# Kernel optimization log

Measured on AMD Instinct MI355X. Metric: run time of the kernel, lower is better.

Reference implementation:

```python
import jax, jax.numpy as jnp
import numpy as np

DIST_THRESHOLD = 900.0  # distance_threshold from __init__
NO_CODE_ID = -1         # no_code_id from __init__


def setup_inputs() -> dict:
    key = jax.random.key(0)
    k1, k2 = jax.random.split(key)
    x = jax.random.normal(k1, (4, 2048, 512), dtype=jnp.float32)      # [b, n, d] tokens
    codes = jax.random.normal(k2, (16384, 512), dtype=jnp.float32)    # [c, d] full codebook
    return {"x": x, "codes": codes}


def reference(x, codes):
    x2 = jnp.sum(x * x, axis=-1, keepdims=True)            # [b, n, 1]
    c2 = jnp.sum(codes * codes, axis=-1)                   # [c]
    xc = jnp.einsum('bnd,cd->bnc', x, codes)               # [b, n, c] (the compute-heavy GEMM)
    dist_sq = jnp.maximum(x2 + c2 - 2.0 * xc, 0.0)         # clamp tiny negatives, like cdist

    within = jnp.any(dist_sq <= DIST_THRESHOLD, axis=-1)   # [b, n]
    nn_ids = jnp.argmin(dist_sq, axis=-1)                  # [b, n]
    ids = jnp.where(within, nn_ids, NO_CODE_ID)            # tokens outside threshold -> no_code_id
    return ids
```

## Files before the change

### kernel.cpp

```cpp
#include <hip/hip_runtime.h>


#define NTOK   8192
#define NCODES 16384
#define DDIM   512
#define NCHUNK 8
#define CHUNK  2048
#define DIST_THR 900.0f

typedef unsigned short u16;
typedef _Float16 half8 __attribute__((ext_vector_type(8)));
typedef float    f32x4 __attribute__((ext_vector_type(4)));

__device__ __forceinline__ void conv_body(const float* __restrict__ src,
                                          u16* __restrict__ dh,
                                          u16* __restrict__ dl, int c) {
    int r = c & 15, q = (c >> 4) & 3, g = (c >> 6) & 7, kit = (c >> 9) & 15;
    int tile = c >> 13;
    int row = tile * 128 + g * 16 + r;
    int k = kit * 32 + q * 8;
    const float* p = src + (size_t)row * DDIM + k;
    float4 v0 = *(const float4*)p;
    float4 v1 = *(const float4*)(p + 4);
    float vv[8] = {v0.x, v0.y, v0.z, v0.w, v1.x, v1.y, v1.z, v1.w};
    u16 hs[8], ls[8];
    #pragma unroll
    for (int j = 0; j < 8; ++j) {
        float sv = vv[j] * 16.0f;
        _Float16 h = (_Float16)sv;
        float hf = (float)h;
        _Float16 l = (_Float16)(sv - hf);
        union { _Float16 f; u16 u; } uh, ul;
        uh.f = h; ul.f = l;
        hs[j] = uh.u; ls[j] = ul.u;
    }
    uint4 H, L;
    H.x = hs[0] | ((unsigned)hs[1] << 16); H.y = hs[2] | ((unsigned)hs[3] << 16);
    H.z = hs[4] | ((unsigned)hs[5] << 16); H.w = hs[6] | ((unsigned)hs[7] << 16);
    L.x = ls[0] | ((unsigned)ls[1] << 16); L.y = ls[2] | ((unsigned)ls[3] << 16);
    L.z = ls[4] | ((unsigned)ls[5] << 16); L.w = ls[6] | ((unsigned)ls[7] << 16);
    *(uint4*)(dh + (size_t)c * 8) = H;
    *(uint4*)(dl + (size_t)c * 8) = L;
}

__global__ __launch_bounds__(256) void nn_prep(const float* __restrict__ x,
                                               const float* __restrict__ codes,
                                               u16* __restrict__ xh, u16* __restrict__ xl,
                                               u16* __restrict__ ch, u16* __restrict__ cl,
                                               float* __restrict__ c2) {
    int b = blockIdx.x;
    if (b < 2048) {
        conv_body(x, xh, xl, b * 256 + threadIdx.x);
    } else if (b < 6144) {
        conv_body(codes, ch, cl, (b - 2048) * 256 + threadIdx.x);
    } else {
        int w = threadIdx.x >> 6;
        int lane = threadIdx.x & 63;
        int c = (b - 6144) * 4 + w;
        const float* p = codes + (size_t)c * DDIM + lane * 8;
        float4 v0 = *(const float4*)p;
        float4 v1 = *(const float4*)(p + 4);
        float s = v0.x*v0.x + v0.y*v0.y + v0.z*v0.z + v0.w*v0.w
                + v1.x*v1.x + v1.y*v1.y + v1.z*v1.z + v1.w*v1.w;
        #pragma unroll
        for (int off = 32; off > 0; off >>= 1) s += __shfl_down(s, off);
        if (lane == 0) c2[c] = s;
    }
}

__global__ __launch_bounds__(512, 2) void nn_gemm(const u16* __restrict__ xh,
                                                  const u16* __restrict__ xl,
                                                  const u16* __restrict__ chh,
                                                  const u16* __restrict__ cll,
                                                  const float* __restrict__ c2,
                                                  float* __restrict__ pmin,
                                                  int* __restrict__ pid) {
    __shared__ __align__(16) char smem[65536];
    const int tid = threadIdx.x;
    const int lane = tid & 63;
    const int wave = tid >> 6;
    const int wm = wave & 3;
    const int wn = wave >> 2;
    const int mtile = blockIdx.x >> 3;
    const int chunk = blockIdx.x & 7;
    const int m0 = mtile * 256;

    const u16* abase_h = xh + (size_t)(mtile * 2 + (wm >> 1)) * 65536
                            + (size_t)((wm & 1) * 4) * 512 + lane * 8;
    const u16* abase_l = xl + (size_t)(mtile * 2 + (wm >> 1)) * 65536
                            + (size_t)((wm & 1) * 4) * 512 + lane * 8;

    const int q = wave >> 2;
    const int s = wave & 3;
    const u16* bsrc = q ? cll : chh;
    const u16* bgbase = bsrc + (size_t)(chunk * 16 + (s >> 1)) * 65536
                             + (size_t)(s & 1) * 2048 + lane * 8;
    const int bldsoff = q * 16384 + (s >> 1) * 8192 + (s & 1) * 4096 + lane * 16;

    float mv[16];
    int   mi[16];
    #pragma unroll
    for (int t = 0; t < 16; ++t) { mv[t] = 3.4e38f; mi[t] = 0; }

    f32x4 acc[4][8];
    #pragma unroll
    for (int i = 0; i < 4; ++i)
        #pragma unroll
        for (int j = 0; j < 8; ++j) acc[i][j] = (f32x4)0.0f;

    auto stage = [&](int it2) {
        int kit2 = it2 & 15, nt2 = it2 >> 4;
        const u16* src = bgbase + (size_t)nt2 * 131072 + (size_t)kit2 * 4096;
        char* dst = smem + (it2 & 1) * 32768 + bldsoff;
        #pragma unroll
        for (int jj = 0; jj < 4; ++jj)
            __builtin_amdgcn_global_load_lds(
                (const __attribute__((address_space(1))) void*)(src + jj * 512),
                (__attribute__((address_space(3))) void*)(dst + jj * 1024),
                16, 0, 0);
    };

    stage(0);
    for (int it = 0; it < 128; ++it) {
        asm volatile("s_waitcnt vmcnt(0)\n\ts_barrier" ::: "memory");

        const char* cur = smem + (it & 1) * 32768;
        const int kit = it & 15;

        half8 ah[4], al[4];
        #pragma unroll
        for (int i = 0; i < 4; ++i) {
            ah[i] = *(const half8*)(abase_h + (size_t)kit * 4096 + i * 512);
            al[i] = *(const half8*)(abase_l + (size_t)kit * 4096 + i * 512);
        }
        if (it < 127) stage(it + 1);

        #pragma unroll
        for (int j = 0; j < 8; ++j) {
            int g = wn * 8 + j;
            half8 bh = *(const half8*)(cur +         g * 1024 + lane * 16);
            half8 bl = *(const half8*)(cur + 16384 + g * 1024 + lane * 16);
            #pragma unroll
            for (int i = 0; i < 4; ++i) {
                acc[i][j] = __builtin_amdgcn_mfma_f32_16x16x32_f16(ah[i], bh, acc[i][j], 0, 0, 0);
                acc[i][j] = __builtin_amdgcn_mfma_f32_16x16x32_f16(ah[i], bl, acc[i][j], 0, 0, 0);
                acc[i][j] = __builtin_amdgcn_mfma_f32_16x16x32_f16(al[i], bh, acc[i][j], 0, 0, 0);
            }
        }

        if ((it & 15) == 15) {
            int nt = it >> 4;
            #pragma unroll
            for (int j = 0; j < 8; ++j) {
                int ncol = nt * 256 + wn * 128 + j * 16 + (lane & 15);
                int gid = chunk * CHUNK + ncol;
                float cv = c2[gid];
                #pragma unroll
                for (int i = 0; i < 4; ++i)
                    #pragma unroll
                    for (int r = 0; r < 4; ++r) {
                        float sc = fmaf(acc[i][j][r], -0.0078125f, cv);
                        int slot = i * 4 + r;
                        if (sc < mv[slot]) { mv[slot] = sc; mi[slot] = gid; }
                    }
            }
            #pragma unroll
            for (int i = 0; i < 4; ++i)
                #pragma unroll
                for (int j = 0; j < 8; ++j) acc[i][j] = (f32x4)0.0f;
        }
    }

    #pragma unroll
    for (int off = 1; off < 16; off <<= 1) {
        #pragma unroll
        for (int t = 0; t < 16; ++t) {
            float ov = __shfl_xor(mv[t], off);
            int   oi = __shfl_xor(mi[t], off);
            if (ov < mv[t] || (ov == mv[t] && oi < mi[t])) { mv[t] = ov; mi[t] = oi; }
        }
    }
    if ((lane & 15) == 0) {
        #pragma unroll
        for (int i = 0; i < 4; ++i)
            #pragma unroll
            for (int r = 0; r < 4; ++r) {
                int row = wm * 64 + i * 16 + (lane >> 4) * 4 + r;
                int2 e;
                e.x = __float_as_int(mv[i * 4 + r]);
                e.y = mi[i * 4 + r];
                *(int2*)(smem + (wn * 256 + row) * 8) = e;
            }
    }
    __syncthreads();
    if (tid < 256) {
        int2 e0 = *(const int2*)(smem + tid * 8);
        int2 e1 = *(const int2*)(smem + (256 + tid) * 8);
        float v0 = __int_as_float(e0.x), v1 = __int_as_float(e1.x);
        float bv = v0; int bi = e0.y;
        if (v1 < bv || (v1 == bv && e1.y < bi)) { bv = v1; bi = e1.y; }
        pmin[(size_t)(m0 + tid) * NCHUNK + chunk] = bv;
        pid [(size_t)(m0 + tid) * NCHUNK + chunk] = bi;
    }
}

__global__ __launch_bounds__(256) void nn_fin(const float* __restrict__ x,
                                              const float* __restrict__ pmin,
                                              const int* __restrict__ pid,
                                              int* __restrict__ out) {
    int w = threadIdx.x >> 6;
    int lane = threadIdx.x & 63;
    int t = blockIdx.x * 4 + w;
    const float* p = x + (size_t)t * DDIM + lane * 8;
    float4 v0 = *(const float4*)p;
    float4 v1 = *(const float4*)(p + 4);
    float s = v0.x*v0.x + v0.y*v0.y + v0.z*v0.z + v0.w*v0.w
            + v1.x*v1.x + v1.y*v1.y + v1.z*v1.z + v1.w*v1.w;
    #pragma unroll
    for (int off = 32; off > 0; off >>= 1) s += __shfl_down(s, off);
    if (lane == 0) {
        const float* pm = pmin + (size_t)t * NCHUNK;
        const int*   pi = pid  + (size_t)t * NCHUNK;
        float bv = pm[0]; int bi = pi[0];
        #pragma unroll
        for (int c = 1; c < NCHUNK; ++c) {
            float v = pm[c]; int id = pi[c];
            if (v < bv || (v == bv && id < bi)) { bv = v; bi = id; }
        }
        float mind = s + bv;
        out[t] = (mind <= DIST_THR) ? bi : -1;
    }
}

extern "C" void kernel_launch(void* const* d_in, const int* in_sizes, int n_in,
                              void* d_out, int out_size, void* d_ws, size_t ws_size,
                              hipStream_t stream) {
    const float* x     = (const float*)d_in[0];
    const float* codes = (const float*)d_in[1];
    int* out = (int*)d_out;

    char* ws = (char*)d_ws;
    u16*   xh   = (u16*)(ws);
    u16*   xl   = (u16*)(ws + 8388608);
    u16*   chh  = (u16*)(ws + 16777216);
    u16*   cll  = (u16*)(ws + 33554432);
    float* c2   = (float*)(ws + 50331648);
    float* pmin = (float*)(ws + 50397184);
    int*   pid  = (int*)  (ws + 50659328);

    nn_prep<<<10240, 256, 0, stream>>>(x, codes, xh, xl, chh, cll, c2);
    nn_gemm<<<32 * NCHUNK, 512, 0, stream>>>(xh, xl, chh, cll, c2, pmin, pid);
    nn_fin<<<NTOK / 4, 256, 0, stream>>>(x, pmin, pid, out);
}
```

Before: 438.1 us.

## Prefetch A fragments across iterations and move running argmin to LDS

Register-double-buffers the A fragments so the next k-step's global loads are issued while the current MFMAs run. B fragments are read from LDS in a two-deep rotation with scheduling barriers to interleave them with MFMAs. The per-lane running min/argmin registers are replaced by a shared-memory table updated after each column tile, which frees registers. The cost is a shuffle reduction every tile instead of once, plus extra LDS.

```diff
diff --git a/kernel.cpp b/kernel.cpp
--- a/kernel.cpp
+++ b/kernel.cpp
@@ -75,7 +75,7 @@
                                                   const float* __restrict__ c2,
                                                   float* __restrict__ pmin,
                                                   int* __restrict__ pid) {
-    __shared__ __align__(16) char smem[65536];
+    __shared__ __align__(16) char smem[69632];
     const int tid = threadIdx.x;
     const int lane = tid & 63;
     const int wave = tid >> 6;
@@ -84,6 +84,12 @@
     const int mtile = blockIdx.x >> 3;
     const int chunk = blockIdx.x & 7;
     const int m0 = mtile * 256;
+    char* tb = smem + 65536;
+
+    if (tid < 512) {
+        int2 e; e.x = __float_as_int(3.4e38f); e.y = 0;
+        *(int2*)(tb + tid * 8) = e;
+    }
 
     const u16* abase_h = xh + (size_t)(mtile * 2 + (wm >> 1)) * 65536
                             + (size_t)((wm & 1) * 4) * 512 + lane * 8;
@@ -97,18 +103,13 @@
                              + (size_t)(s & 1) * 2048 + lane * 8;
     const int bldsoff = q * 16384 + (s >> 1) * 8192 + (s & 1) * 4096 + lane * 16;
 
-    float mv[16];
-    int   mi[16];
-    #pragma unroll
-    for (int t = 0; t < 16; ++t) { mv[t] = 3.4e38f; mi[t] = 0; }
-
     f32x4 acc[4][8];
     #pragma unroll
     for (int i = 0; i < 4; ++i)
         #pragma unroll
         for (int j = 0; j < 8; ++j) acc[i][j] = (f32x4)0.0f;
 
-    auto stage = [&](int it2) {
+    auto stageB = [&](int it2) {
         int kit2 = it2 & 15, nt2 = it2 >> 4;
         const u16* src = bgbase + (size_t)nt2 * 131072 + (size_t)kit2 * 4096;
         char* dst = smem + (it2 & 1) * 32768 + bldsoff;
@@ -119,83 +120,103 @@
                 (__attribute__((address_space(3))) void*)(dst + jj * 1024),
                 16, 0, 0);
     };
-
-    stage(0);
-    for (int it = 0; it < 128; ++it) {
-        asm volatile("s_waitcnt vmcnt(0)\n\ts_barrier" ::: "memory");
-
-        const char* cur = smem + (it & 1) * 32768;
-        const int kit = it & 15;
-
-        half8 ah[4], al[4];
+    auto loadA = [&](int it2, half8 (&h)[4], half8 (&l)[4]) {
+        int kit2 = it2 & 15;
         #pragma unroll
         for (int i = 0; i < 4; ++i) {
-            ah[i] = *(const half8*)(abase_h + (size_t)kit * 4096 + i * 512);
-            al[i] = *(const half8*)(abase_l + (size_t)kit * 4096 + i * 512);
-        }
-        if (it < 127) stage(it + 1);
-
+            h[i] = *(const half8*)(abase_h + (size_t)kit2 * 4096 + i * 512);
+            l[i] = *(const half8*)(abase_l + (size_t)kit2 * 4096 + i * 512);
+        }
+    };
+
+    auto epilogue = [&](int it, f32x4 (&a)[4][8]) {
+        int nt = it >> 4;
+        float mvs[16]; int mis[16];
+        #pragma unroll
+        for (int t = 0; t < 16; ++t) { mvs[t] = 3.4e38f; mis[t] = 0; }
         #pragma unroll
         for (int j = 0; j < 8; ++j) {
-            int g = wn * 8 + j;
-            half8 bh = *(const half8*)(cur +         g * 1024 + lane * 16);
-            half8 bl = *(const half8*)(cur + 16384 + g * 1024 + lane * 16);
-            #pragma unroll
-            for (int i = 0; i < 4; ++i) {
-                acc[i][j] = __builtin_amdgcn_mfma_f32_16x16x32_f16(ah[i], bh, acc[i][j], 0, 0, 0);
-                acc[i][j] = __builtin_amdgcn_mfma_f32_16x16x32_f16(ah[i], bl, acc[i][j], 0, 0, 0);
-                acc[i][j] = __builtin_amdgcn_mfma_f32_16x16x32_f16(al[i], bh, acc[i][j], 0, 0, 0);
-            }
-        }
-
-        if ((it & 15) == 15) {
-            int nt = it >> 4;
-            #pragma unroll
-            for (int j = 0; j < 8; ++j) {
-                int ncol = nt * 256 + wn * 128 + j * 16 + (lane & 15);
-                int gid = chunk * CHUNK + ncol;
-                float cv = c2[gid];
-                #pragma unroll
-                for (int i = 0; i < 4; ++i)
-                    #pragma unroll
-                    for (int r = 0; r < 4; ++r) {
-                        float sc = fmaf(acc[i][j][r], -0.0078125f, cv);
-                        int slot = i * 4 + r;
-                        if (sc < mv[slot]) { mv[slot] = sc; mi[slot] = gid; }
-                    }
-            }
+            int ncol = nt * 256 + wn * 128 + j * 16 + (lane & 15);
+            int gid = chunk * CHUNK + ncol;
+            float cv = c2[gid];
             #pragma unroll
             for (int i = 0; i < 4; ++i)
                 #pragma unroll
-                for (int j = 0; j < 8; ++j) acc[i][j] = (f32x4)0.0f;
-        }
-    }
-
-    #pragma unroll
-    for (int off = 1; off < 16; off <<= 1) {
-        #pragma unroll
-        for (int t = 0; t < 16; ++t) {
-            float ov = __shfl_xor(mv[t], off);
-            int   oi = __shfl_xor(mi[t], off);
-            if (ov < mv[t] || (ov == mv[t] && oi < mi[t])) { mv[t] = ov; mi[t] = oi; }
-        }
-    }
-    if ((lane & 15) == 0) {
+                for (int r = 0; r < 4; ++r) {
+                    float sc = fmaf(a[i][j][r], -0.0078125f, cv);
+                    int slot = i * 4 + r;
+                    if (sc < mvs[slot]) { mvs[slot] = sc; mis[slot] = gid; }
+                }
+        }
+        #pragma unroll
+        for (int off = 1; off < 16; off <<= 1) {
+            #pragma unroll
+            for (int t = 0; t < 16; ++t) {
+                float ov = __shfl_xor(mvs[t], off);
+                int   oi = __shfl_xor(mis[t], off);
+                if (ov < mvs[t] || (ov == mvs[t] && oi < mis[t])) { mvs[t] = ov; mis[t] = oi; }
+            }
+        }
+        if ((lane & 15) == 0) {
+            #pragma unroll
+            for (int t = 0; t < 16; ++t) {
+                int row = wm * 64 + (t >> 2) * 16 + (lane >> 4) * 4 + (t & 3);
+                int2* e = (int2*)(tb + (wn * 256 + row) * 8);
+                if (mvs[t] < __int_as_float(e->x)) {
+                    int2 w2; w2.x = __float_as_int(mvs[t]); w2.y = mis[t];
+                    *e = w2;
+                }
+            }
+        }
         #pragma unroll
         for (int i = 0; i < 4; ++i)
             #pragma unroll
-            for (int r = 0; r < 4; ++r) {
-                int row = wm * 64 + i * 16 + (lane >> 4) * 4 + r;
-                int2 e;
-                e.x = __float_as_int(mv[i * 4 + r]);
-                e.y = mi[i * 4 + r];
-                *(int2*)(smem + (wn * 256 + row) * 8) = e;
-            }
-    }
+            for (int j = 0; j < 8; ++j) a[i][j] = (f32x4)0.0f;
+    };
+
+    auto body = [&](int it, half8 (&cah)[4], half8 (&cal)[4],
+                    half8 (&nah)[4], half8 (&nal)[4]) {
+        asm volatile("s_waitcnt vmcnt(0)\n\ts_barrier" ::: "memory");
+        const char* cur = smem + (it & 1) * 32768;
+        if (it < 127) { stageB(it + 1); loadA(it + 1, nah, nal); }
+
+        half8 bbh[2], bbl[2];
+        bbh[0] = *(const half8*)(cur +         (wn * 8 + 0) * 1024 + lane * 16);
+        bbl[0] = *(const half8*)(cur + 16384 + (wn * 8 + 0) * 1024 + lane * 16);
+        bbh[1] = *(const half8*)(cur +         (wn * 8 + 1) * 1024 + lane * 16);
+        bbl[1] = *(const half8*)(cur + 16384 + (wn * 8 + 1) * 1024 + lane * 16);
+
+        #pragma unroll
+        for (int j = 0; j < 8; ++j) {
+            half8 bh = bbh[j & 1], bl = bbl[j & 1];
+            #pragma unroll
+            for (int i = 0; i < 4; ++i) {
+                acc[i][j] = __builtin_amdgcn_mfma_f32_16x16x32_f16(cah[i], bh, acc[i][j], 0, 0, 0);
+                acc[i][j] = __builtin_amdgcn_mfma_f32_16x16x32_f16(cah[i], bl, acc[i][j], 0, 0, 0);
+                acc[i][j] = __builtin_amdgcn_mfma_f32_16x16x32_f16(cal[i], bh, acc[i][j], 0, 0, 0);
+            }
+            if (j < 6) {
+                int g = wn * 8 + j + 2;
+                bbh[j & 1] = *(const half8*)(cur +         g * 1024 + lane * 16);
+                bbl[j & 1] = *(const half8*)(cur + 16384 + g * 1024 + lane * 16);
+                __builtin_amdgcn_sched_barrier(0);
+            }
+        }
+        if ((it & 15) == 15) epilogue(it, acc);
+    };
+
+    half8 aXh[4], aXl[4], aYh[4], aYl[4];
+    stageB(0);
+    loadA(0, aXh, aXl);
+    for (int it2 = 0; it2 < 64; ++it2) {
+        body(2 * it2,     aXh, aXl, aYh, aYl);
+        body(2 * it2 + 1, aYh, aYl, aXh, aXl);
+    }
+
     __syncthreads();
     if (tid < 256) {
-        int2 e0 = *(const int2*)(smem + tid * 8);
-        int2 e1 = *(const int2*)(smem + (256 + tid) * 8);
+        int2 e0 = *(const int2*)(tb + tid * 8);
+        int2 e1 = *(const int2*)(tb + (256 + tid) * 8);
         float v0 = __int_as_float(e0.x), v1 = __int_as_float(e1.x);
         float bv = v0; int bi = e0.y;
         if (v1 < bv || (v1 == bv && e1.y < bi)) { bv = v1; bi = e1.y; }
```

New measurement: 459.8 us. +5.0%, slower.
